# Kernel tuning notes

Measured on AMD Instinct MI355X. Metric: run time of the kernel, lower is better.

## Reference

```python
import jax, jax.numpy as jnp
import numpy as np

B, AT, NBR = 8, 96, 512
NG, NT = 25, 5            # n_gaussian_triple, n_theta
NANG = NG * NT            # 125, filternet input dim
NF = 128                  # n_filters
NB = 128                  # n_atom_basis


def ssp(x):
    # shifted softplus: ln(0.5*e^x + 0.5) = softplus(x) - ln(2)
    return jax.nn.softplus(x) - jnp.asarray(np.log(2.0), x.dtype)


def setup_inputs() -> dict:
    key = jax.random.key(0)
    ks = jax.random.split(key, 16)
    s = lambda fan_in: 1.0 / np.sqrt(fan_in)
    return {
        "x": jax.random.normal(ks[0], (B, AT, NB), jnp.float32),
        "triple_ijk": jax.random.uniform(ks[1], (B, AT, NBR, NANG), jnp.float32),
        "neighbors_j": jax.random.randint(ks[2], (B, AT, NBR), 0, AT, jnp.int32),
        "neighbors_k": jax.random.randint(ks[3], (B, AT, NBR), 0, AT, jnp.int32),
        "triple_mask": jnp.ones((B, AT, NBR), jnp.float32),
        # filter network (Dense ssp -> Dense linear)
        "W1": jax.random.normal(ks[4], (NANG, NF), jnp.float32) * s(NANG),
        "b1": jnp.zeros((NF,), jnp.float32),
        "W2": jax.random.normal(ks[5], (NF, NF), jnp.float32) * s(NF),
        "b2": jnp.zeros((NF,), jnp.float32),
        # cfconv in2f (no bias) and f2out (ssp activation)
        "Win": jax.random.normal(ks[6], (NB, NF), jnp.float32) * s(NB),
        "Wf2": jax.random.normal(ks[7], (NF, NB), jnp.float32) * s(NF),
        "bf2": jnp.zeros((NB,), jnp.float32),
        # final dense (linear) before residual
        "Wd": jax.random.normal(ks[8], (NB, NB), jnp.float32) * s(NB),
        "bd": jnp.zeros((NB,), jnp.float32),
    }


def _gather_atoms(y, nbh):
    # y: (B, At, F); nbh: (B, At, Nbr) -> (B, At, Nbr, F)
    b, at, nbr = nbh.shape
    idx = nbh.reshape(b, at * nbr, 1)
    return jnp.take_along_axis(y, idx, axis=1).reshape(b, at, nbr, y.shape[-1])


def reference(x, triple_ijk, neighbors_j, neighbors_k, triple_mask,
              W1, b1, W2, b2, Win, Wf2, bf2, Wd, bd):
    # filter network on angular/radial triple features -> (B, At, Nbr, NF)
    W_triple = ssp(triple_ijk @ W1 + b1) @ W2 + b2
    # in2f
    y = x @ Win                                  # (B, At, NF)
    y_j = _gather_atoms(y, neighbors_j)          # (B, At, Nbr, NF)
    y_k = _gather_atoms(y, neighbors_k)          # (B, At, Nbr, NF)
    # element-wise continuous-filter conv over triples, mask padded triples
    yt = y_j * y_k * W_triple * triple_mask[..., None]
    agg = jnp.sum(yt, axis=2)                    # sum-aggregate over triples
    v = ssp(agg @ Wf2 + bf2)                     # f2out with shifted softplus
    v = v @ Wd + bd                              # interaction dense
    return x + v                                 # residual
```

## Files before the change

### kernel.cpp

```cpp
#include <hip/hip_runtime.h>
#include <math.h>

#define B_    8
#define AT_   96
#define NBR_  512
#define NANG_ 125
#define NF_   128
#define NB_   128
#define TN    32
#define NCHUNK 2
#define CROWS (NBR_ / NCHUNK)
#define NTI   (CROWS / TN)
#define YSTRIDE 36

typedef __attribute__((ext_vector_type(8))) short bf16x8;
typedef __attribute__((ext_vector_type(4))) float f32x4;
typedef __attribute__((ext_vector_type(4))) unsigned u32x4;

__device__ __forceinline__ short f2bf(float f) {
    union { float f; unsigned u; } x; x.f = f;
    return (short)((x.u + 0x8000u) >> 16);
}

__device__ __forceinline__ float sspf(float x) {
    float p = __builtin_amdgcn_exp2f(x * 1.44269504088896340736f);
    float l = __builtin_amdgcn_logf(1.0f + p);
    return 0.69314718055994530942f * l - 0.69314718055994530942f;
}

__device__ __forceinline__ void load_tile(const float* __restrict__ tile,
                                          int row, int seg, float* v) {
    const float* s = tile + row * NANG_ + seg * 16;
    if (seg < 7) {
        #pragma unroll
        for (int j = 0; j < 16; j++) v[j] = s[j];
    } else {
        #pragma unroll
        for (int j = 0; j < 13; j++) v[j] = s[j];
        v[13] = 0.f; v[14] = 0.f; v[15] = 0.f;
    }
}

__device__ __forceinline__ void store_tile(short* dst, int row, int seg, const float* v) {
    unsigned r[8];
    #pragma unroll
    for (int i = 0; i < 8; i++) {
        unsigned x;
        asm("v_cvt_pk_bf16_f32 %0, %1, %2" : "=v"(x) : "v"(v[2 * i]), "v"(v[2 * i + 1]));
        r[i] = x;
    }
    const int swz = (row & 7) << 4;
    char* base = (char*)dst + row * 256;
    *(u32x4*)(base + ((seg * 32) ^ swz))      = (u32x4){r[0], r[1], r[2], r[3]};
    *(u32x4*)(base + ((seg * 32 + 16) ^ swz)) = (u32x4){r[4], r[5], r[6], r[7]};
}

__global__ __launch_bounds__(128) void prep_kernel(
    const float* __restrict__ x, const float* __restrict__ Win,
    const float* __restrict__ W1, const float* __restrict__ W2,
    float* __restrict__ y, short* __restrict__ w1p, short* __restrict__ w2p)
{
    __shared__ float xs[4][NB_];
    int blk = blockIdx.x, tid = threadIdx.x;
    if (blk < 192) {
        int row0 = blk * 4;
        #pragma unroll
        for (int r = 0; r < 4; r++) xs[r][tid] = x[(row0 + r) * NB_ + tid];
        __syncthreads();
        float a0 = 0.f, a1 = 0.f, a2 = 0.f, a3 = 0.f;
        #pragma unroll 8
        for (int k = 0; k < NB_; k++) {
            float w = Win[k * NF_ + tid];
            a0 = fmaf(xs[0][k], w, a0);
            a1 = fmaf(xs[1][k], w, a1);
            a2 = fmaf(xs[2][k], w, a2);
            a3 = fmaf(xs[3][k], w, a3);
        }
        y[(row0 + 0) * NF_ + tid] = a0;
        y[(row0 + 1) * NF_ + tid] = a1;
        y[(row0 + 2) * NF_ + tid] = a2;
        y[(row0 + 3) * NF_ + tid] = a3;
    } else {
        int t = (blk - 192) * 128 + tid;
        int j = t & 7, lane = (t >> 3) & 63, ks = (t >> 9) & 3, ct = t >> 11;
        int k = ks * 32 + (lane >> 4) * 8 + j;
        int n = ct * 16 + (lane & 15);
        w1p[t] = (k < NANG_) ? f2bf(W1[k * NF_ + n]) : (short)0;
        w2p[t] = f2bf(W2[k * NF_ + n]);
    }
}

__global__ __launch_bounds__(256, 3) void triple_partial(
    const float* __restrict__ trip,
    const int* __restrict__ nbj, const int* __restrict__ nbk,
    const float* __restrict__ maskg,
    const float* __restrict__ b1g, const float* __restrict__ b2g,
    const float* __restrict__ y, const short* __restrict__ w1p,
    const short* __restrict__ w2p, float* __restrict__ pagg)
{
    __shared__ short tileT[2][TN * 128];
    __shared__ short hs[2][TN * 128];
    __shared__ float yjkw[4][TN * YSTRIDE];

    const int tid = threadIdx.x;
    const int wave = tid >> 6, lane = tid & 63;
    const int quad = lane >> 4, col = lane & 15;
    const int blk = blockIdx.x;
    const int bid = blk >> 1, c = blk & 1;
    const int b = bid / AT_;

    const float* tpc = trip + (long)bid * NBR_ * NANG_ + (long)c * CROWS * NANG_;
    const int nb_base = bid * NBR_ + c * CROWS;

    const int ct0 = 2 * wave, ct1 = 2 * wave + 1;
    const int f0 = ct0 * 16 + col, f1 = ct1 * 16 + col;
    const float bias1_0 = b1g[f0], bias1_1 = b1g[f1];
    const float bias2_0 = b2g[f0], bias2_1 = b2g[f1];

    const int trow = tid >> 3, tseg = tid & 7;
    const int row2 = lane >> 1, h = lane & 1;
    const int ycol = wave * 32 + h * 16;
    const int swzA = (col & 7) << 4;
    const int quad16 = quad * 16;

    bf16x8 w1f0[4], w1f1[4], w2f0[4], w2f1[4];
    #pragma unroll
    for (int ks = 0; ks < 4; ks++) {
        w1f0[ks] = *(const bf16x8*)&w1p[(ct0 * 4 + ks) * 512 + lane * 8];
        w1f1[ks] = *(const bf16x8*)&w1p[(ct1 * 4 + ks) * 512 + lane * 8];
        w2f0[ks] = *(const bf16x8*)&w2p[(ct0 * 4 + ks) * 512 + lane * 8];
        w2f1[ks] = *(const bf16x8*)&w2p[(ct1 * 4 + ks) * 512 + lane * 8];
    }

    float v[16];
    load_tile(tpc, trow, tseg, v);
    int jj = nbj[nb_base + row2];
    int kk = nbk[nb_base + row2];
    float mk = maskg[nb_base + row2];
    store_tile(&tileT[0][0], trow, tseg, v);
    __syncthreads();

    float accw0 = 0.f, accw1 = 0.f;
    int cur = 0;

    for (int nt = 0; nt < NTI; nt++) {
        if (nt + 1 < NTI)
            load_tile(tpc + (nt + 1) * (TN * NANG_), trow, tseg, v);

        const float* yj = y + (b * AT_ + jj) * NF_ + ycol;
        const float* yk = y + (b * AT_ + kk) * NF_ + ycol;
        f32x4 j0 = ((const f32x4*)yj)[0], j1 = ((const f32x4*)yj)[1];
        f32x4 j2 = ((const f32x4*)yj)[2], j3 = ((const f32x4*)yj)[3];
        f32x4 k0 = ((const f32x4*)yk)[0], k1 = ((const f32x4*)yk)[1];
        f32x4 k2 = ((const f32x4*)yk)[2], k3 = ((const f32x4*)yk)[3];
        const float mc = mk;
        if (nt + 1 < NTI) {
            jj = nbj[nb_base + (nt + 1) * TN + row2];
            kk = nbk[nb_base + (nt + 1) * TN + row2];
            mk = maskg[nb_base + (nt + 1) * TN + row2];
        }

        const char* tbA = (const char*)&tileT[cur][0] + col * 256;
        const char* tbB = (const char*)&tileT[cur][0] + (16 + col) * 256;
        f32x4 d00 = {0,0,0,0}, d01 = {0,0,0,0}, d10 = {0,0,0,0}, d11 = {0,0,0,0};
        #pragma unroll
        for (int ks = 0; ks < 4; ks++) {
            const int off = (ks * 64 + quad16) ^ swzA;
            bf16x8 a0 = *(const bf16x8*)(tbA + off);
            bf16x8 a1 = *(const bf16x8*)(tbB + off);
            d00 = __builtin_amdgcn_mfma_f32_16x16x32_bf16(a0, w1f0[ks], d00, 0, 0, 0);
            d01 = __builtin_amdgcn_mfma_f32_16x16x32_bf16(a0, w1f1[ks], d01, 0, 0, 0);
            d10 = __builtin_amdgcn_mfma_f32_16x16x32_bf16(a1, w1f0[ks], d10, 0, 0, 0);
            d11 = __builtin_amdgcn_mfma_f32_16x16x32_bf16(a1, w1f1[ks], d11, 0, 0, 0);
        }

        {
            float* d = &yjkw[wave][row2 * YSTRIDE + h * 16];
            *(f32x4*)(d + 0)  = j0 * k0 * mc;
            *(f32x4*)(d + 4)  = j1 * k1 * mc;
            *(f32x4*)(d + 8)  = j2 * k2 * mc;
            *(f32x4*)(d + 12) = j3 * k3 * mc;
        }
        {
            char* hw = (char*)&hs[cur][0];
            #pragma unroll
            for (int r = 0; r < 4; r++) {
                int row0 = quad * 4 + r, row1 = row0 + 16;
                int s0 = (row0 & 7) << 4;
                *(short*)(hw + row0 * 256 + ((2 * f0) ^ s0)) = f2bf(sspf(d00[r] + bias1_0));
                *(short*)(hw + row0 * 256 + ((2 * f1) ^ s0)) = f2bf(sspf(d01[r] + bias1_1));
                *(short*)(hw + row1 * 256 + ((2 * f0) ^ s0)) = f2bf(sspf(d10[r] + bias1_0));
                *(short*)(hw + row1 * 256 + ((2 * f1) ^ s0)) = f2bf(sspf(d11[r] + bias1_1));
            }
        }
        if (nt + 1 < NTI)
            store_tile(&tileT[cur ^ 1][0], trow, tseg, v);

        __syncthreads();

        const char* hbA = (const char*)&hs[cur][0] + col * 256;
        const char* hbB = (const char*)&hs[cur][0] + (16 + col) * 256;
        f32x4 e00 = {0,0,0,0}, e01 = {0,0,0,0}, e10 = {0,0,0,0}, e11 = {0,0,0,0};
        #pragma unroll
        for (int ks = 0; ks < 4; ks++) {
            const int off = (ks * 64 + quad16) ^ swzA;
            bf16x8 a0 = *(const bf16x8*)(hbA + off);
            bf16x8 a1 = *(const bf16x8*)(hbB + off);
            e00 = __builtin_amdgcn_mfma_f32_16x16x32_bf16(a0, w2f0[ks], e00, 0, 0, 0);
            e01 = __builtin_amdgcn_mfma_f32_16x16x32_bf16(a0, w2f1[ks], e01, 0, 0, 0);
            e10 = __builtin_amdgcn_mfma_f32_16x16x32_bf16(a1, w2f0[ks], e10, 0, 0, 0);
            e11 = __builtin_amdgcn_mfma_f32_16x16x32_bf16(a1, w2f1[ks], e11, 0, 0, 0);
        }
        const float* yw = &yjkw[wave][0];
        #pragma unroll
        for (int r = 0; r < 4; r++) {
            int row0 = quad * 4 + r, row1 = row0 + 16;
            accw0 += (e00[r] + bias2_0) * yw[row0 * YSTRIDE + col];
            accw1 += (e01[r] + bias2_1) * yw[row0 * YSTRIDE + col + 16];
            accw0 += (e10[r] + bias2_0) * yw[row1 * YSTRIDE + col];
            accw1 += (e11[r] + bias2_1) * yw[row1 * YSTRIDE + col + 16];
        }
        cur ^= 1;
    }

    accw0 += __shfl_xor(accw0, 16, 64);
    accw0 += __shfl_xor(accw0, 32, 64);
    accw1 += __shfl_xor(accw1, 16, 64);
    accw1 += __shfl_xor(accw1, 32, 64);
    if (quad == 0) {
        pagg[blk * NF_ + f0] = accw0;
        pagg[blk * NF_ + f1] = accw1;
    }
}

__global__ __launch_bounds__(128) void finish_kernel(
    const float* __restrict__ x, const float* __restrict__ pagg,
    const float* __restrict__ Wf2, const float* __restrict__ bf2,
    const float* __restrict__ Wd, const float* __restrict__ bd,
    float* __restrict__ out)
{
    __shared__ float aggs[NF_];
    __shared__ float t1s[NF_];
    int bid = blockIdx.x, f = threadIdx.x;
    float a = pagg[(bid * 2 + 0) * NF_ + f] + pagg[(bid * 2 + 1) * NF_ + f];
    aggs[f] = a;
    __syncthreads();
    float acc = 0.f;
    #pragma unroll 8
    for (int k = 0; k < NF_; k++) acc = fmaf(aggs[k], Wf2[k * NB_ + f], acc);
    t1s[f] = sspf(acc + bf2[f]);
    __syncthreads();
    acc = 0.f;
    #pragma unroll 8
    for (int k = 0; k < NB_; k++) acc = fmaf(t1s[k], Wd[k * NB_ + f], acc);
    out[bid * NB_ + f] = x[bid * NB_ + f] + acc + bd[f];
}

extern "C" void kernel_launch(void* const* d_in, const int* in_sizes, int n_in,
                              void* d_out, int out_size, void* d_ws, size_t ws_size,
                              hipStream_t stream) {
    const float* x    = (const float*)d_in[0];
    const float* trip = (const float*)d_in[1];
    const int*   nbj  = (const int*)d_in[2];
    const int*   nbk  = (const int*)d_in[3];
    const float* mask = (const float*)d_in[4];
    const float* W1   = (const float*)d_in[5];
    const float* b1   = (const float*)d_in[6];
    const float* W2   = (const float*)d_in[7];
    const float* b2   = (const float*)d_in[8];
    const float* Win  = (const float*)d_in[9];
    const float* Wf2  = (const float*)d_in[10];
    const float* bf2  = (const float*)d_in[11];
    const float* Wd   = (const float*)d_in[12];
    const float* bd   = (const float*)d_in[13];
    float* out = (float*)d_out;

    char* ws = (char*)d_ws;
    float* y    = (float*)ws;
    short* w1p  = (short*)(ws + 393216);
    short* w2p  = (short*)(ws + 393216 + 32768);
    float* pagg = (float*)(ws + 393216 + 65536);

    prep_kernel<<<320, 128, 0, stream>>>(x, Win, W1, W2, y, w1p, w2p);
    triple_partial<<<B_ * AT_ * NCHUNK, 256, 0, stream>>>(trip, nbj, nbk, mask,
        b1, b2, y, w1p, w2p, pagg);
    finish_kernel<<<B_ * AT_, 128, 0, stream>>>(x, pagg, Wf2, bf2, Wd, bd, out);
}
```

Before: 352.1 us.

## Prefetch neighbor gathers one tile ahead, store yjk in bf16, reload W2 per tile

```diff
diff --git a/kernel.cpp b/kernel.cpp
--- a/kernel.cpp
+++ b/kernel.cpp
@@ -11,7 +11,7 @@
 #define NCHUNK 2
 #define CROWS (NBR_ / NCHUNK)
 #define NTI   (CROWS / TN)
-#define YSTRIDE 36
+#define YSTB  40
 
 typedef __attribute__((ext_vector_type(8))) short bf16x8;
 typedef __attribute__((ext_vector_type(4))) float f32x4;
@@ -20,6 +20,11 @@
 __device__ __forceinline__ short f2bf(float f) {
     union { float f; unsigned u; } x; x.f = f;
     return (short)((x.u + 0x8000u) >> 16);
+}
+
+__device__ __forceinline__ float bf2f(unsigned short u) {
+    union { unsigned u; float f; } x; x.u = ((unsigned)u) << 16;
+    return x.f;
 }
 
 __device__ __forceinline__ float sspf(float x) {
@@ -28,9 +33,16 @@
     return 0.69314718055994530942f * l - 0.69314718055994530942f;
 }
 
-__device__ __forceinline__ void load_tile(const float* __restrict__ tile,
-                                          int row, int seg, float* v) {
+__device__ __forceinline__ unsigned cvtpk(float lo, float hi) {
+    unsigned r;
+    asm("v_cvt_pk_bf16_f32 %0, %1, %2" : "=v"(r) : "v"(lo), "v"(hi));
+    return r;
+}
+
+__device__ __forceinline__ void load_cvt(const float* __restrict__ tile,
+                                         int row, int seg, unsigned* r) {
     const float* s = tile + row * NANG_ + seg * 16;
+    float v[16];
     if (seg < 7) {
         #pragma unroll
         for (int j = 0; j < 16; j++) v[j] = s[j];
@@ -39,16 +51,12 @@
         for (int j = 0; j < 13; j++) v[j] = s[j];
         v[13] = 0.f; v[14] = 0.f; v[15] = 0.f;
     }
-}
-
-__device__ __forceinline__ void store_tile(short* dst, int row, int seg, const float* v) {
-    unsigned r[8];
     #pragma unroll
-    for (int i = 0; i < 8; i++) {
-        unsigned x;
-        asm("v_cvt_pk_bf16_f32 %0, %1, %2" : "=v"(x) : "v"(v[2 * i]), "v"(v[2 * i + 1]));
-        r[i] = x;
-    }
+    for (int i = 0; i < 8; i++) r[i] = cvtpk(v[2 * i], v[2 * i + 1]);
+}
+
+__device__ __forceinline__ void store_swz(short* dst, int row, int seg,
+                                          const unsigned* r) {
     const int swz = (row & 7) << 4;
     char* base = (char*)dst + row * 256;
     *(u32x4*)(base + ((seg * 32) ^ swz))      = (u32x4){r[0], r[1], r[2], r[3]};
@@ -100,7 +108,7 @@
 {
     __shared__ short tileT[2][TN * 128];
     __shared__ short hs[2][TN * 128];
-    __shared__ float yjkw[4][TN * YSTRIDE];
+    __shared__ unsigned short yjkw[4][TN * YSTB];
 
     const int tid = threadIdx.x;
     const int wave = tid >> 6, lane = tid & 63;
@@ -123,21 +131,31 @@
     const int swzA = (col & 7) << 4;
     const int quad16 = quad * 16;
 
-    bf16x8 w1f0[4], w1f1[4], w2f0[4], w2f1[4];
+    bf16x8 w1f0[4], w1f1[4];
     #pragma unroll
     for (int ks = 0; ks < 4; ks++) {
         w1f0[ks] = *(const bf16x8*)&w1p[(ct0 * 4 + ks) * 512 + lane * 8];
         w1f1[ks] = *(const bf16x8*)&w1p[(ct1 * 4 + ks) * 512 + lane * 8];
-        w2f0[ks] = *(const bf16x8*)&w2p[(ct0 * 4 + ks) * 512 + lane * 8];
-        w2f1[ks] = *(const bf16x8*)&w2p[(ct1 * 4 + ks) * 512 + lane * 8];
-    }
-
-    float v[16];
-    load_tile(tpc, trow, tseg, v);
-    int jj = nbj[nb_base + row2];
-    int kk = nbk[nb_base + row2];
-    float mk = maskg[nb_base + row2];
-    store_tile(&tileT[0][0], trow, tseg, v);
+    }
+
+    int jn = nbj[nb_base + row2], kn = nbk[nb_base + row2];
+    float mcur = maskg[nb_base + row2];
+    f32x4 gj0, gj1, gj2, gj3, gk0, gk1, gk2, gk3;
+    {
+        const float* yj = y + (b * AT_ + jn) * NF_ + ycol;
+        const float* yk = y + (b * AT_ + kn) * NF_ + ycol;
+        gj0 = ((const f32x4*)yj)[0]; gj1 = ((const f32x4*)yj)[1];
+        gj2 = ((const f32x4*)yj)[2]; gj3 = ((const f32x4*)yj)[3];
+        gk0 = ((const f32x4*)yk)[0]; gk1 = ((const f32x4*)yk)[1];
+        gk2 = ((const f32x4*)yk)[2]; gk3 = ((const f32x4*)yk)[3];
+    }
+    jn = nbj[nb_base + TN + row2];
+    kn = nbk[nb_base + TN + row2];
+    float mn = maskg[nb_base + TN + row2];
+
+    unsigned stg[8];
+    load_cvt(tpc, trow, tseg, stg);
+    store_swz(&tileT[0][0], trow, tseg, stg);
     __syncthreads();
 
     float accw0 = 0.f, accw1 = 0.f;
@@ -145,20 +163,7 @@
 
     for (int nt = 0; nt < NTI; nt++) {
         if (nt + 1 < NTI)
-            load_tile(tpc + (nt + 1) * (TN * NANG_), trow, tseg, v);
-
-        const float* yj = y + (b * AT_ + jj) * NF_ + ycol;
-        const float* yk = y + (b * AT_ + kk) * NF_ + ycol;
-        f32x4 j0 = ((const f32x4*)yj)[0], j1 = ((const f32x4*)yj)[1];
-        f32x4 j2 = ((const f32x4*)yj)[2], j3 = ((const f32x4*)yj)[3];
-        f32x4 k0 = ((const f32x4*)yk)[0], k1 = ((const f32x4*)yk)[1];
-        f32x4 k2 = ((const f32x4*)yk)[2], k3 = ((const f32x4*)yk)[3];
-        const float mc = mk;
-        if (nt + 1 < NTI) {
-            jj = nbj[nb_base + (nt + 1) * TN + row2];
-            kk = nbk[nb_base + (nt + 1) * TN + row2];
-            mk = maskg[nb_base + (nt + 1) * TN + row2];
-        }
+            load_cvt(tpc + (nt + 1) * (TN * NANG_), trow, tseg, stg);
 
         const char* tbA = (const char*)&tileT[cur][0] + col * 256;
         const char* tbB = (const char*)&tileT[cur][0] + (16 + col) * 256;
@@ -175,11 +180,15 @@
         }
 
         {
-            float* d = &yjkw[wave][row2 * YSTRIDE + h * 16];
-            *(f32x4*)(d + 0)  = j0 * k0 * mc;
-            *(f32x4*)(d + 4)  = j1 * k1 * mc;
-            *(f32x4*)(d + 8)  = j2 * k2 * mc;
-            *(f32x4*)(d + 12) = j3 * k3 * mc;
+            f32x4 p0 = gj0 * gk0 * mcur, p1 = gj1 * gk1 * mcur;
+            f32x4 p2 = gj2 * gk2 * mcur, p3 = gj3 * gk3 * mcur;
+            unsigned y0 = cvtpk(p0.x, p0.y), y1 = cvtpk(p0.z, p0.w);
+            unsigned y2 = cvtpk(p1.x, p1.y), y3 = cvtpk(p1.z, p1.w);
+            unsigned y4 = cvtpk(p2.x, p2.y), y5 = cvtpk(p2.z, p2.w);
+            unsigned y6 = cvtpk(p3.x, p3.y), y7 = cvtpk(p3.z, p3.w);
+            unsigned short* d = &yjkw[wave][row2 * YSTB + h * 16];
+            *(u32x4*)(d)     = (u32x4){y0, y1, y2, y3};
+            *(u32x4*)(d + 8) = (u32x4){y4, y5, y6, y7};
         }
         {
             char* hw = (char*)&hs[cur][0];
@@ -193,8 +202,14 @@
                 *(short*)(hw + row1 * 256 + ((2 * f1) ^ s0)) = f2bf(sspf(d11[r] + bias1_1));
             }
         }
+        bf16x8 w2f0[4], w2f1[4];
+        #pragma unroll
+        for (int ks = 0; ks < 4; ks++) {
+            w2f0[ks] = *(const bf16x8*)&w2p[(ct0 * 4 + ks) * 512 + lane * 8];
+            w2f1[ks] = *(const bf16x8*)&w2p[(ct1 * 4 + ks) * 512 + lane * 8];
+        }
         if (nt + 1 < NTI)
-            store_tile(&tileT[cur ^ 1][0], trow, tseg, v);
+            store_swz(&tileT[cur ^ 1][0], trow, tseg, stg);
 
         __syncthreads();
 
@@ -211,14 +226,29 @@
             e10 = __builtin_amdgcn_mfma_f32_16x16x32_bf16(a1, w2f0[ks], e10, 0, 0, 0);
             e11 = __builtin_amdgcn_mfma_f32_16x16x32_bf16(a1, w2f1[ks], e11, 0, 0, 0);
         }
-        const float* yw = &yjkw[wave][0];
+        const unsigned short* yw = &yjkw[wave][0];
         #pragma unroll
         for (int r = 0; r < 4; r++) {
             int row0 = quad * 4 + r, row1 = row0 + 16;
-            accw0 += (e00[r] + bias2_0) * yw[row0 * YSTRIDE + col];
-            accw1 += (e01[r] + bias2_1) * yw[row0 * YSTRIDE + col + 16];
-            accw0 += (e10[r] + bias2_0) * yw[row1 * YSTRIDE + col];
-            accw1 += (e11[r] + bias2_1) * yw[row1 * YSTRIDE + col + 16];
+            accw0 += (e00[r] + bias2_0) * bf2f(yw[row0 * YSTB + col]);
+            accw1 += (e01[r] + bias2_1) * bf2f(yw[row0 * YSTB + col + 16]);
+            accw0 += (e10[r] + bias2_0) * bf2f(yw[row1 * YSTB + col]);
+            accw1 += (e11[r] + bias2_1) * bf2f(yw[row1 * YSTB + col + 16]);
+        }
+
+        if (nt + 1 < NTI) {
+            const float* yj = y + (b * AT_ + jn) * NF_ + ycol;
+            const float* yk = y + (b * AT_ + kn) * NF_ + ycol;
+            gj0 = ((const f32x4*)yj)[0]; gj1 = ((const f32x4*)yj)[1];
+            gj2 = ((const f32x4*)yj)[2]; gj3 = ((const f32x4*)yj)[3];
+            gk0 = ((const f32x4*)yk)[0]; gk1 = ((const f32x4*)yk)[1];
+            gk2 = ((const f32x4*)yk)[2]; gk3 = ((const f32x4*)yk)[3];
+            mcur = mn;
+            if (nt + 2 < NTI) {
+                jn = nbj[nb_base + (nt + 2) * TN + row2];
+                kn = nbk[nb_base + (nt + 2) * TN + row2];
+                mn = maskg[nb_base + (nt + 2) * TN + row2];
+            }
         }
         cur ^= 1;
     }
```

Measured after the change: 354.7 us. No clear change (+0.8%).
